# Performance work log

Measured on AMD Instinct MI355X. Metric: run time of the kernel, lower is better.

Reference implementation:

```python
import jax, jax.numpy as jnp
import numpy as np

D = 2048          # n_embd
F = 1408          # moe_inter_dim
E = 8             # n_routed_experts
TOPK = 2          # n_activated_experts
N_SHARED = 2
ROUTE_SCALE = 1.0


def setup_inputs() -> dict:
    key = jax.random.key(0)
    ks = jax.random.split(key, 8)
    s = 0.02
    x = jax.random.normal(ks[0], (2, 1024, D), dtype=jnp.float32)
    gate_w = jax.random.normal(ks[1], (D, E), dtype=jnp.float32) * s
    Fs = F * N_SHARED
    sw1 = jax.random.normal(ks[2], (D, Fs), dtype=jnp.float32) * s
    sw2 = jax.random.normal(ks[3], (Fs, D), dtype=jnp.float32) * s
    sw3 = jax.random.normal(ks[4], (D, Fs), dtype=jnp.float32) * s
    rw1 = jax.random.normal(ks[5], (E, D, F), dtype=jnp.float32) * s
    rw2 = jax.random.normal(ks[6], (E, F, D), dtype=jnp.float32) * s
    rw3 = jax.random.normal(ks[7], (E, D, F), dtype=jnp.float32) * s
    return {"x": x, "gate_w": gate_w, "sw1": sw1, "sw2": sw2, "sw3": sw3,
            "rw1": rw1, "rw2": rw2, "rw3": rw3}


def _swiglu(x, w1, w2, w3):
    return (jax.nn.silu(x @ w1) * (x @ w3)) @ w2


def reference(x, gate_w, sw1, sw2, sw3, rw1, rw2, rw3):
    B, T, _ = x.shape
    xf = x.reshape(-1, D)                       # [N, D]
    N = xf.shape[0]
    # shared experts (always applied)
    y = _swiglu(xf, sw1, sw2, sw3)              # [N, D]
    # gate: softmax scores, top-k (bias is None since n_embd != 7168; n_groups == 1)
    scores = jax.nn.softmax(xf @ gate_w, axis=-1)       # [N, E]
    weights, indices = jax.lax.top_k(scores, TOPK)       # gathered original scores
    weights = weights * ROUTE_SCALE
    # combine weights per (token, expert); zero for unassigned -> same math as
    # the per-expert gather/scatter loop in the original module
    cw = jnp.zeros((N, E), dtype=xf.dtype).at[jnp.arange(N)[:, None], indices].add(weights)
    for e in range(E):  # fixed small structural loop over experts
        h = _swiglu(xf, rw1[e], rw2[e], rw3[e])  # [N, D]
        y = y + cw[:, e:e + 1] * h
    return y.reshape(B, T, D)
```

## Files before the change

kernel.cpp:

```cpp
#include <hip/hip_runtime.h>
#include <hip/hip_bf16.h>
#include <math.h>

#define D_DIM 2048
#define F_DIM 1408
#define FS_DIM 2816
#define E_NUM 8
#define N_TOK 2048

typedef __attribute__((ext_vector_type(8))) short bf16x8;
typedef __attribute__((ext_vector_type(4))) float f32x4;

#define WAITVM(n) asm volatile("s_waitcnt vmcnt(" #n ")" ::: "memory")

__device__ inline short f2bf(float f) {
    __hip_bfloat16 h = __float2bfloat16(f);
    return *reinterpret_cast<short*>(&h);
}
__device__ inline float bf2f(short s) {
    __hip_bfloat16 h; *reinterpret_cast<short*>(&h) = s;
    return __bfloat162float(h);
}
__device__ inline float silu1(float v) { return v / (1.f + expf(-v)); }

__device__ inline void async_copy16(const void* g, void* l) {
    __builtin_amdgcn_global_load_lds(
        (const __attribute__((address_space(1))) void*)g,
        (__attribute__((address_space(3))) void*)l, 16, 0, 0);
}

__device__ inline void t64h(const float* in, short* out, int K, int N,
                            int kt, int nt, float (*tile)[65], int t)
{
    int k0 = kt * 64, n0 = nt * 64;
    int tr = t >> 4, tc4 = (t & 15) * 4;
#pragma unroll
    for (int i = 0; i < 4; ++i) {
        int r = tr + i * 16;
        float4 v = *reinterpret_cast<const float4*>(in + (size_t)(k0 + r) * N + n0 + tc4);
        tile[r][tc4 + 0] = v.x; tile[r][tc4 + 1] = v.y;
        tile[r][tc4 + 2] = v.z; tile[r][tc4 + 3] = v.w;
    }
    __syncthreads();
#pragma unroll
    for (int i = 0; i < 4; ++i) {
        int n = tr + i * 16;
        short4 s4;
        s4.x = f2bf(tile[tc4 + 0][n]);
        s4.y = f2bf(tile[tc4 + 1][n]);
        s4.z = f2bf(tile[tc4 + 2][n]);
        s4.w = f2bf(tile[tc4 + 3][n]);
        *reinterpret_cast<short4*>(out + (size_t)(n0 + n) * K + k0 + tc4) = s4;
    }
}

__global__ __launch_bounds__(256) void prep_kernel(
    const float* __restrict__ x, const float* __restrict__ gw,
    float* __restrict__ assign_w, int* __restrict__ expert_count,
    int* __restrict__ expert_list, short* __restrict__ Xb,
    const float* __restrict__ sw1, short* __restrict__ swt1,
    const float* __restrict__ sw3, short* __restrict__ swt3,
    const float* __restrict__ rw1, short* __restrict__ rwt1,
    const float* __restrict__ rw3, short* __restrict__ rwt3)
{
    __shared__ float tile[64][65];
    int bid = blockIdx.x;
    int tid = threadIdx.x;
    if (bid < 512) {
        int wid = bid * 4 + (tid >> 6);
        int lane = tid & 63;
        const float* xr = x + (size_t)wid * D_DIM;
        float p[E_NUM];
#pragma unroll
        for (int e = 0; e < E_NUM; ++e) p[e] = 0.f;
        for (int d = lane; d < D_DIM; d += 64) {
            float xv = xr[d];
            const float4* g = reinterpret_cast<const float4*>(gw + (size_t)d * E_NUM);
            float4 g0 = g[0], g1 = g[1];
            p[0] = fmaf(xv, g0.x, p[0]); p[1] = fmaf(xv, g0.y, p[1]);
            p[2] = fmaf(xv, g0.z, p[2]); p[3] = fmaf(xv, g0.w, p[3]);
            p[4] = fmaf(xv, g1.x, p[4]); p[5] = fmaf(xv, g1.y, p[5]);
            p[6] = fmaf(xv, g1.z, p[6]); p[7] = fmaf(xv, g1.w, p[7]);
        }
#pragma unroll
        for (int off = 32; off > 0; off >>= 1)
#pragma unroll
            for (int e = 0; e < E_NUM; ++e)
                p[e] += __shfl_xor(p[e], off, 64);
        if (lane == 0) {
            float m = p[0];
#pragma unroll
            for (int e = 1; e < E_NUM; ++e) m = fmaxf(m, p[e]);
            float s = 0.f, pr[E_NUM];
#pragma unroll
            for (int e = 0; e < E_NUM; ++e) { pr[e] = expf(p[e] - m); s += pr[e]; }
            float inv = 1.f / s;
#pragma unroll
            for (int e = 0; e < E_NUM; ++e) pr[e] *= inv;
            int i0 = 0;
#pragma unroll
            for (int e = 1; e < E_NUM; ++e) if (pr[e] > pr[i0]) i0 = e;
            int i1 = (i0 == 0) ? 1 : 0;
#pragma unroll
            for (int e = 0; e < E_NUM; ++e) if (e != i0 && pr[e] > pr[i1]) i1 = e;
            int s0 = wid * 2, s1 = wid * 2 + 1;
            assign_w[s0] = pr[i0];
            assign_w[s1] = pr[i1];
            int p0 = atomicAdd(&expert_count[i0], 1);
            expert_list[i0 * N_TOK + p0] = s0;
            int p1 = atomicAdd(&expert_count[i1], 1);
            expert_list[i1 * N_TOK + p1] = s1;
        }
    } else if (bid < 2560) {
        int i = ((bid - 512) * 256 + tid) * 8;
        float4 v0 = *reinterpret_cast<const float4*>(x + i);
        float4 v1 = *reinterpret_cast<const float4*>(x + i + 4);
        bf16x8 o;
        o[0] = f2bf(v0.x); o[1] = f2bf(v0.y); o[2] = f2bf(v0.z); o[3] = f2bf(v0.w);
        o[4] = f2bf(v1.x); o[5] = f2bf(v1.y); o[6] = f2bf(v1.z); o[7] = f2bf(v1.w);
        *reinterpret_cast<bf16x8*>(Xb + i) = o;
    } else if (bid < 3968) {
        int t = bid - 2560;
        t64h(sw1, swt1, D_DIM, FS_DIM, t % 32, t / 32, tile, tid);
    } else if (bid < 5376) {
        int t = bid - 3968;
        t64h(sw3, swt3, D_DIM, FS_DIM, t % 32, t / 32, tile, tid);
    } else if (bid < 11008) {
        int t = bid - 5376;
        int e = t / 704, r = t % 704;
        t64h(rw1 + (size_t)e * D_DIM * F_DIM, rwt1 + (size_t)e * F_DIM * D_DIM,
             D_DIM, F_DIM, r % 32, r / 32, tile, tid);
    } else {
        int t = bid - 11008;
        int e = t / 704, r = t % 704;
        t64h(rw3 + (size_t)e * D_DIM * F_DIM, rwt3 + (size_t)e * F_DIM * D_DIM,
             D_DIM, F_DIM, r % 32, r / 32, tile, tid);
    }
}

__global__ __launch_bounds__(512) void moe_in_kernel(
    const short* __restrict__ Xb,
    const short* __restrict__ swt1, const short* __restrict__ swt3, short* __restrict__ Hs,
    const short* __restrict__ rwt1, const short* __restrict__ rwt3, short* __restrict__ Hr,
    const int* __restrict__ expert_list, const int* __restrict__ expert_count,
    const float* __restrict__ sw2, short* __restrict__ swt2,
    const float* __restrict__ rw2, short* __restrict__ rwt2)
{
    __shared__ char SMEM[131072];
    int bid = blockIdx.x, tid = threadIdx.x;

    if (bid >= 896) {
        int t2 = (bid - 896) * 2 + (tid >> 8);
        int t256 = tid & 255;
        float (*tile)[65] = reinterpret_cast<float (*)[65]>(SMEM + (tid >> 8) * 16640);
        if (t2 < 1408) {
            t64h(sw2, swt2, FS_DIM, D_DIM, t2 % 44, t2 / 44, tile, t256);
        } else {
            int r = t2 - 1408;
            int e = r / 704, rr = r % 704;
            t64h(rw2 + (size_t)e * F_DIM * D_DIM, rwt2 + (size_t)e * D_DIM * F_DIM,
                 F_DIM, D_DIM, rr % 22, rr / 22, tile, t256);
        }
        return;
    }

    int xcd = bid & 7, qq = bid >> 3, mtile = qq & 7, gq = qq >> 3;
    int g = gq * 8 + xcd;
    if (g >= 110) return;
    bool gather;
    const short *W1, *W3;
    short* H;
    int ldH, n0, count;
    const int* list = nullptr;
    int m0 = mtile * 256;
    if (g < 22) {
        gather = false; count = N_TOK;
        W1 = swt1; W3 = swt3; H = Hs; ldH = FS_DIM; n0 = g * 128;
    } else {
        int g2 = g - 22, e = g2 / 11;
        n0 = (g2 % 11) * 128;
        gather = true;
        count = expert_count[e];
        if (m0 >= count) return;
        list = expert_list + e * N_TOK;
        W1 = rwt1 + (size_t)e * F_DIM * D_DIM;
        W3 = rwt3 + (size_t)e * F_DIM * D_DIM;
        H = Hr; ldH = F_DIM;
    }

    int l = tid & 63, w = tid >> 6;

    const char* aS[4];
#pragma unroll
    for (int j = 0; j < 4; ++j) {
        int u = j * 512 + tid, r = u >> 3, s = u & 7;
        int rr = m0 + r;
        int tok = gather ? ((rr < count) ? (list[rr] >> 1) : 0) : rr;
        aS[j] = (const char*)Xb + (size_t)tok * 4096 + ((s ^ (r & 7)) << 4);
    }
    const char *b1S[2], *b3S[2];
#pragma unroll
    for (int j = 0; j < 2; ++j) {
        int u = j * 512 + tid, r = u >> 3, s = u & 7;
        size_t off = (size_t)(n0 + r) * 4096 + ((s ^ (r & 7)) << 4);
        b1S[j] = (const char*)W1 + off;
        b3S[j] = (const char*)W3 + off;
    }

    auto STAGE = [&](int buf, int kb) {
        char* base = SMEM + buf * 65536;
#pragma unroll
        for (int j = 0; j < 4; ++j)
            async_copy16(aS[j] + kb, base + (j * 512 + tid) * 16);
#pragma unroll
        for (int j = 0; j < 2; ++j) {
            async_copy16(b1S[j] + kb, base + 32768 + (j * 512 + tid) * 16);
            async_copy16(b3S[j] + kb, base + 49152 + (j * 512 + tid) * 16);
        }
    };

    int wm = w >> 1, wn = w & 1, frow = l & 15, fkg = l >> 4;
    f32x4 acc1[4][4], acc3[4][4];
#pragma unroll
    for (int i = 0; i < 4; ++i)
#pragma unroll
        for (int j = 0; j < 4; ++j) { acc1[i][j] = (f32x4)0.f; acc3[i][j] = (f32x4)0.f; }

    STAGE(0, 0);
    int buf = 0;
    for (int it = 0; it < 32; ++it) {
        if (it < 31) { STAGE(buf ^ 1, (it + 1) << 7); WAITVM(8); }
        else         { WAITVM(0); }
        __builtin_amdgcn_s_barrier();
        const char* base = SMEM + buf * 65536;
#pragma unroll
        for (int kk = 0; kk < 2; ++kk) {
            bf16x8 af[4], b1f[4], b3f[4];
#pragma unroll
            for (int mf = 0; mf < 4; ++mf) {
                int r = wm * 64 + mf * 16 + frow;
                af[mf] = *reinterpret_cast<const bf16x8*>(
                    base + r * 128 + ((((kk << 2) | fkg) ^ (r & 7)) << 4));
            }
#pragma unroll
            for (int nf = 0; nf < 4; ++nf) {
                int r = wn * 64 + nf * 16 + frow;
                int so = (((kk << 2) | fkg) ^ (r & 7)) << 4;
                b1f[nf] = *reinterpret_cast<const bf16x8*>(base + 32768 + r * 128 + so);
                b3f[nf] = *reinterpret_cast<const bf16x8*>(base + 49152 + r * 128 + so);
            }
#pragma unroll
            for (int mf = 0; mf < 4; ++mf)
#pragma unroll
                for (int nf = 0; nf < 4; ++nf) {
                    acc1[mf][nf] = __builtin_amdgcn_mfma_f32_16x16x32_bf16(
                        af[mf], b1f[nf], acc1[mf][nf], 0, 0, 0);
                    acc3[mf][nf] = __builtin_amdgcn_mfma_f32_16x16x32_bf16(
                        af[mf], b3f[nf], acc3[mf][nf], 0, 0, 0);
                }
        }
        __builtin_amdgcn_s_barrier();
        buf ^= 1;
    }

#pragma unroll
    for (int mf = 0; mf < 4; ++mf) {
#pragma unroll
        for (int jj = 0; jj < 4; ++jj) {
            int rl = wm * 64 + mf * 16 + fkg * 4 + jj;
            int rr = m0 + rl;
            int s;
            if (gather) { if (rr >= count) continue; s = list[rr]; }
            else s = rr;
            short* hp = H + (size_t)s * ldH + n0 + wn * 64 + frow;
#pragma unroll
            for (int nf = 0; nf < 4; ++nf)
                hp[nf * 16] = f2bf(silu1(acc1[mf][nf][jj]) * acc3[mf][nf][jj]);
        }
    }
}

__global__ __launch_bounds__(512) void moe_out_kernel(
    const short* __restrict__ Hs, const short* __restrict__ swt2, float* __restrict__ Y,
    const short* __restrict__ Hr, const short* __restrict__ rwt2, short* __restrict__ H2,
    const int* __restrict__ expert_list, const int* __restrict__ expert_count)
{
    __shared__ char SMEM[98304];
    int bid = blockIdx.x, tid = threadIdx.x;
    int xcd = bid & 7, qq = bid >> 3, mtile = qq & 7, gq = qq >> 3;
    int g = gq * 8 + xcd;
    if (g >= 144) return;
    bool gather;
    const short *A, *B;
    int ldKb, NIT, n0, count;
    const int* list = nullptr;
    int m0 = mtile * 256;
    if (g < 16) {
        gather = false; count = N_TOK;
        A = Hs; ldKb = FS_DIM * 2; NIT = 44; B = swt2; n0 = g * 128;
    } else {
        int g2 = g - 16, e = g2 >> 4;
        n0 = (g2 & 15) * 128;
        gather = true;
        count = expert_count[e];
        if (m0 >= count) return;
        list = expert_list + e * N_TOK;
        A = Hr; ldKb = F_DIM * 2; NIT = 22;
        B = rwt2 + (size_t)e * D_DIM * F_DIM;
    }

    int l = tid & 63, w = tid >> 6;

    const char* aS[4];
#pragma unroll
    for (int j = 0; j < 4; ++j) {
        int u = j * 512 + tid, r = u >> 3, s = u & 7;
        int rr = m0 + r;
        int arow = gather ? ((rr < count) ? list[rr] : 0) : rr;
        aS[j] = (const char*)A + (size_t)arow * ldKb + ((s ^ (r & 7)) << 4);
    }
    const char* bS[2];
#pragma unroll
    for (int j = 0; j < 2; ++j) {
        int u = j * 512 + tid, r = u >> 3, s = u & 7;
        bS[j] = (const char*)B + (size_t)(n0 + r) * ldKb + ((s ^ (r & 7)) << 4);
    }

    auto STAGE = [&](int buf, int kb) {
        char* base = SMEM + buf * 49152;
#pragma unroll
        for (int j = 0; j < 4; ++j)
            async_copy16(aS[j] + kb, base + (j * 512 + tid) * 16);
#pragma unroll
        for (int j = 0; j < 2; ++j)
            async_copy16(bS[j] + kb, base + 32768 + (j * 512 + tid) * 16);
    };

    int wm = w >> 1, wn = w & 1, frow = l & 15, fkg = l >> 4;
    f32x4 acc[4][4];
#pragma unroll
    for (int i = 0; i < 4; ++i)
#pragma unroll
        for (int j = 0; j < 4; ++j) acc[i][j] = (f32x4)0.f;

    STAGE(0, 0);
    int buf = 0;
    for (int it = 0; it < NIT; ++it) {
        if (it + 1 < NIT) { STAGE(buf ^ 1, (it + 1) << 7); WAITVM(6); }
        else              { WAITVM(0); }
        __builtin_amdgcn_s_barrier();
        const char* base = SMEM + buf * 49152;
#pragma unroll
        for (int kk = 0; kk < 2; ++kk) {
            bf16x8 af[4], bf[4];
#pragma unroll
            for (int mf = 0; mf < 4; ++mf) {
                int r = wm * 64 + mf * 16 + frow;
                af[mf] = *reinterpret_cast<const bf16x8*>(
                    base + r * 128 + ((((kk << 2) | fkg) ^ (r & 7)) << 4));
            }
#pragma unroll
            for (int nf = 0; nf < 4; ++nf) {
                int r = wn * 64 + nf * 16 + frow;
                bf[nf] = *reinterpret_cast<const bf16x8*>(
                    base + 32768 + r * 128 + ((((kk << 2) | fkg) ^ (r & 7)) << 4));
            }
#pragma unroll
            for (int mf = 0; mf < 4; ++mf)
#pragma unroll
                for (int nf = 0; nf < 4; ++nf)
                    acc[mf][nf] = __builtin_amdgcn_mfma_f32_16x16x32_bf16(
                        af[mf], bf[nf], acc[mf][nf], 0, 0, 0);
        }
        __builtin_amdgcn_s_barrier();
        buf ^= 1;
    }

#pragma unroll
    for (int mf = 0; mf < 4; ++mf) {
#pragma unroll
        for (int jj = 0; jj < 4; ++jj) {
            int rl = wm * 64 + mf * 16 + fkg * 4 + jj;
            int rr = m0 + rl;
            int s;
            if (gather) { if (rr >= count) continue; s = list[rr]; }
            else s = rr;
            int col = n0 + wn * 64 + frow;
            if (!gather) {
                float* op = Y + (size_t)s * D_DIM + col;
#pragma unroll
                for (int nf = 0; nf < 4; ++nf)
                    op[nf * 16] = acc[mf][nf][jj];
            } else {
                short* op = H2 + (size_t)s * D_DIM + col;
#pragma unroll
                for (int nf = 0; nf < 4; ++nf)
                    op[nf * 16] = f2bf(acc[mf][nf][jj]);
            }
        }
    }
}

__global__ __launch_bounds__(256) void combine_kernel(
    float* __restrict__ Y, const short* __restrict__ H2,
    const float* __restrict__ assign_w)
{
    int tok = blockIdx.x, tid = threadIdx.x;
    float w0 = assign_w[2 * tok];
    float w1 = assign_w[2 * tok + 1];
    const short* h0 = H2 + (size_t)(2 * tok) * D_DIM + tid * 8;
    const short* h1 = h0 + D_DIM;
    bf16x8 a = *reinterpret_cast<const bf16x8*>(h0);
    bf16x8 b = *reinterpret_cast<const bf16x8*>(h1);
    float* y = Y + (size_t)tok * D_DIM + tid * 8;
    float4 y0 = *reinterpret_cast<float4*>(y);
    float4 y1 = *reinterpret_cast<float4*>(y + 4);
    y0.x = fmaf(w0, bf2f(a[0]), fmaf(w1, bf2f(b[0]), y0.x));
    y0.y = fmaf(w0, bf2f(a[1]), fmaf(w1, bf2f(b[1]), y0.y));
    y0.z = fmaf(w0, bf2f(a[2]), fmaf(w1, bf2f(b[2]), y0.z));
    y0.w = fmaf(w0, bf2f(a[3]), fmaf(w1, bf2f(b[3]), y0.w));
    y1.x = fmaf(w0, bf2f(a[4]), fmaf(w1, bf2f(b[4]), y1.x));
    y1.y = fmaf(w0, bf2f(a[5]), fmaf(w1, bf2f(b[5]), y1.y));
    y1.z = fmaf(w0, bf2f(a[6]), fmaf(w1, bf2f(b[6]), y1.z));
    y1.w = fmaf(w0, bf2f(a[7]), fmaf(w1, bf2f(b[7]), y1.w));
    *reinterpret_cast<float4*>(y) = y0;
    *reinterpret_cast<float4*>(y + 4) = y1;
}

extern "C" void kernel_launch(void* const* d_in, const int* in_sizes, int n_in,
                              void* d_out, int out_size, void* d_ws, size_t ws_size,
                              hipStream_t stream) {
    const float* x   = (const float*)d_in[0];
    const float* gw  = (const float*)d_in[1];
    const float* sw1 = (const float*)d_in[2];
    const float* sw2 = (const float*)d_in[3];
    const float* sw3 = (const float*)d_in[4];
    const float* rw1 = (const float*)d_in[5];
    const float* rw2 = (const float*)d_in[6];
    const float* rw3 = (const float*)d_in[7];
    float* Y = (float*)d_out;

    char* ws = (char*)d_ws;
    float* assign_w     = (float*)(ws);
    int*   expert_count = (int*)(ws + 16384);
    int*   expert_list  = (int*)(ws + 16384 + 256);

    const size_t XB_OFF   = 131072;
    const size_t SWT1_OFF = XB_OFF + 8388608ull;
    const size_t SWT3_OFF = SWT1_OFF + 11534336ull;
    const size_t SWT2_OFF = SWT3_OFF + 11534336ull;
    const size_t RWT1_OFF = SWT2_OFF + 11534336ull;
    const size_t RWT3_OFF = RWT1_OFF + 46137344ull;
    const size_t RWT2_OFF = RWT3_OFF + 46137344ull;
    const size_t HS_OFF   = RWT2_OFF + 46137344ull;
    const size_t HR_OFF   = HS_OFF + 11534336ull;
    const size_t H2_OFF   = HR_OFF + 11534336ull;

    short* Xb   = (short*)(ws + XB_OFF);
    short* swt1 = (short*)(ws + SWT1_OFF);
    short* swt3 = (short*)(ws + SWT3_OFF);
    short* swt2 = (short*)(ws + SWT2_OFF);
    short* rwt1 = (short*)(ws + RWT1_OFF);
    short* rwt3 = (short*)(ws + RWT3_OFF);
    short* rwt2 = (short*)(ws + RWT2_OFF);
    short* Hs   = (short*)(ws + HS_OFF);
    short* Hr   = (short*)(ws + HR_OFF);
    short* H2   = (short*)(ws + H2_OFF);

    hipMemsetAsync(expert_count, 0, E_NUM * sizeof(int), stream);

    prep_kernel<<<16640, 256, 0, stream>>>(
        x, gw, assign_w, expert_count, expert_list, Xb,
        sw1, swt1, sw3, swt3, rw1, rwt1, rw3, rwt3);

    moe_in_kernel<<<4416, 512, 0, stream>>>(
        Xb, swt1, swt3, Hs, rwt1, rwt3, Hr,
        expert_list, expert_count, sw2, swt2, rw2, rwt2);

    moe_out_kernel<<<1152, 512, 0, stream>>>(
        Hs, swt2, Y, Hr, rwt2, H2, expert_list, expert_count);

    combine_kernel<<<N_TOK, 256, 0, stream>>>(Y, H2, assign_w);
}
```

Before: 391.3 us.

## Switch MoE GEMMs to 4-stage K=32 pipeline with split-phase async loads

Both the gate/up and down-projection kernels move from a double-buffered K=64 loop to a four-buffer ring with K=32 steps and three stages prefetched ahead. Each step is split into two halves separated by a barrier, and the next stage's loads are issued between them so copies overlap the MFMA work. Warps are rearranged into a 2x4 grid of 128x32 subtiles, which changes the LDS fragment reuse pattern. s_setprio raises wave priority around the MFMA blocks. The aim is to hide global-load latency better, at the cost of twice as many barriers per unit of K and smaller LDS rows with a 4-way swizzle that may raise bank conflicts.

```diff
diff --git a/kernel.cpp b/kernel.cpp
--- a/kernel.cpp
+++ b/kernel.cpp
@@ -189,92 +189,99 @@
     }
 
     int l = tid & 63, w = tid >> 6;
-
-    const char* aS[4];
-#pragma unroll
-    for (int j = 0; j < 4; ++j) {
-        int u = j * 512 + tid, r = u >> 3, s = u & 7;
+    int wm = w >> 2, wn = w & 3, frow = l & 15, fkg = l >> 4;
+
+    const char* aS[2];
+#pragma unroll
+    for (int j = 0; j < 2; ++j) {
+        int u = j * 512 + tid, r = u >> 2, s = u & 3;
         int rr = m0 + r;
         int tok = gather ? ((rr < count) ? (list[rr] >> 1) : 0) : rr;
-        aS[j] = (const char*)Xb + (size_t)tok * 4096 + ((s ^ (r & 7)) << 4);
-    }
-    const char *b1S[2], *b3S[2];
-#pragma unroll
-    for (int j = 0; j < 2; ++j) {
-        int u = j * 512 + tid, r = u >> 3, s = u & 7;
-        size_t off = (size_t)(n0 + r) * 4096 + ((s ^ (r & 7)) << 4);
-        b1S[j] = (const char*)W1 + off;
-        b3S[j] = (const char*)W3 + off;
-    }
-
-    auto STAGE = [&](int buf, int kb) {
-        char* base = SMEM + buf * 65536;
-#pragma unroll
-        for (int j = 0; j < 4; ++j)
-            async_copy16(aS[j] + kb, base + (j * 512 + tid) * 16);
-#pragma unroll
-        for (int j = 0; j < 2; ++j) {
-            async_copy16(b1S[j] + kb, base + 32768 + (j * 512 + tid) * 16);
-            async_copy16(b3S[j] + kb, base + 49152 + (j * 512 + tid) * 16);
-        }
-    };
-
-    int wm = w >> 1, wn = w & 1, frow = l & 15, fkg = l >> 4;
-    f32x4 acc1[4][4], acc3[4][4];
-#pragma unroll
-    for (int i = 0; i < 4; ++i)
-#pragma unroll
-        for (int j = 0; j < 4; ++j) { acc1[i][j] = (f32x4)0.f; acc3[i][j] = (f32x4)0.f; }
-
-    STAGE(0, 0);
-    int buf = 0;
-    for (int it = 0; it < 32; ++it) {
-        if (it < 31) { STAGE(buf ^ 1, (it + 1) << 7); WAITVM(8); }
-        else         { WAITVM(0); }
+        aS[j] = (const char*)Xb + (size_t)tok * 4096 + ((s ^ (r & 3)) << 4);
+    }
+    int brr = tid >> 2, bss = tid & 3;
+    size_t boff = (size_t)(n0 + brr) * 4096 + ((bss ^ (brr & 3)) << 4);
+    const char* b1S = (const char*)W1 + boff;
+    const char* b3S = (const char*)W3 + boff;
+
+    f32x4 acc1[8][2], acc3[8][2];
+#pragma unroll
+    for (int i = 0; i < 8; ++i)
+#pragma unroll
+        for (int j = 0; j < 2; ++j) { acc1[i][j] = (f32x4)0.f; acc3[i][j] = (f32x4)0.f; }
+
+#pragma unroll
+    for (int p = 0; p < 3; ++p) {
+        char* base = SMEM + p * 32768;
+        int kb = p << 6;
+        async_copy16(aS[0] + kb, base + tid * 16);
+        async_copy16(aS[1] + kb, base + (512 + tid) * 16);
+        async_copy16(b1S + kb, base + 16384 + tid * 16);
+        async_copy16(b3S + kb, base + 24576 + tid * 16);
+    }
+
+    for (int t = 0; t < 64; ++t) {
+        const char* base = SMEM + (t & 3) * 32768;
+        int ts = (t + 3 < 64) ? (t + 3) : 63;
+        char* sbase = SMEM + ((t + 3) & 3) * 32768;
+        int skb = ts << 6;
+        WAITVM(8);
         __builtin_amdgcn_s_barrier();
-        const char* base = SMEM + buf * 65536;
-#pragma unroll
-        for (int kk = 0; kk < 2; ++kk) {
-            bf16x8 af[4], b1f[4], b3f[4];
-#pragma unroll
-            for (int mf = 0; mf < 4; ++mf) {
-                int r = wm * 64 + mf * 16 + frow;
-                af[mf] = *reinterpret_cast<const bf16x8*>(
-                    base + r * 128 + ((((kk << 2) | fkg) ^ (r & 7)) << 4));
-            }
-#pragma unroll
-            for (int nf = 0; nf < 4; ++nf) {
-                int r = wn * 64 + nf * 16 + frow;
-                int so = (((kk << 2) | fkg) ^ (r & 7)) << 4;
-                b1f[nf] = *reinterpret_cast<const bf16x8*>(base + 32768 + r * 128 + so);
-                b3f[nf] = *reinterpret_cast<const bf16x8*>(base + 49152 + r * 128 + so);
-            }
-#pragma unroll
-            for (int mf = 0; mf < 4; ++mf)
-#pragma unroll
-                for (int nf = 0; nf < 4; ++nf) {
-                    acc1[mf][nf] = __builtin_amdgcn_mfma_f32_16x16x32_bf16(
-                        af[mf], b1f[nf], acc1[mf][nf], 0, 0, 0);
-                    acc3[mf][nf] = __builtin_amdgcn_mfma_f32_16x16x32_bf16(
-                        af[mf], b3f[nf], acc3[mf][nf], 0, 0, 0);
-                }
-        }
+        bf16x8 af[8], bf[2];
+#pragma unroll
+        for (int mf = 0; mf < 8; ++mf) {
+            int r = wm * 128 + mf * 16 + frow;
+            af[mf] = *reinterpret_cast<const bf16x8*>(
+                base + r * 64 + ((fkg ^ (r & 3)) << 4));
+        }
+#pragma unroll
+        for (int nf = 0; nf < 2; ++nf) {
+            int rb = wn * 32 + nf * 16 + frow;
+            bf[nf] = *reinterpret_cast<const bf16x8*>(
+                base + 16384 + rb * 64 + ((fkg ^ (rb & 3)) << 4));
+        }
+        async_copy16(aS[0] + skb, sbase + tid * 16);
+        async_copy16(aS[1] + skb, sbase + (512 + tid) * 16);
+        __builtin_amdgcn_s_setprio(1);
+#pragma unroll
+        for (int mf = 0; mf < 8; ++mf)
+#pragma unroll
+            for (int nf = 0; nf < 2; ++nf)
+                acc1[mf][nf] = __builtin_amdgcn_mfma_f32_16x16x32_bf16(
+                    af[mf], bf[nf], acc1[mf][nf], 0, 0, 0);
+        __builtin_amdgcn_s_setprio(0);
         __builtin_amdgcn_s_barrier();
-        buf ^= 1;
-    }
-
-#pragma unroll
-    for (int mf = 0; mf < 4; ++mf) {
+#pragma unroll
+        for (int nf = 0; nf < 2; ++nf) {
+            int rb = wn * 32 + nf * 16 + frow;
+            bf[nf] = *reinterpret_cast<const bf16x8*>(
+                base + 24576 + rb * 64 + ((fkg ^ (rb & 3)) << 4));
+        }
+        async_copy16(b1S + skb, sbase + 16384 + tid * 16);
+        async_copy16(b3S + skb, sbase + 24576 + tid * 16);
+        __builtin_amdgcn_s_setprio(1);
+#pragma unroll
+        for (int mf = 0; mf < 8; ++mf)
+#pragma unroll
+            for (int nf = 0; nf < 2; ++nf)
+                acc3[mf][nf] = __builtin_amdgcn_mfma_f32_16x16x32_bf16(
+                    af[mf], bf[nf], acc3[mf][nf], 0, 0, 0);
+        __builtin_amdgcn_s_setprio(0);
+    }
+    WAITVM(0);
+
+#pragma unroll
+    for (int mf = 0; mf < 8; ++mf) {
 #pragma unroll
         for (int jj = 0; jj < 4; ++jj) {
-            int rl = wm * 64 + mf * 16 + fkg * 4 + jj;
+            int rl = wm * 128 + mf * 16 + fkg * 4 + jj;
             int rr = m0 + rl;
             int s;
             if (gather) { if (rr >= count) continue; s = list[rr]; }
             else s = rr;
-            short* hp = H + (size_t)s * ldH + n0 + wn * 64 + frow;
-#pragma unroll
-            for (int nf = 0; nf < 4; ++nf)
+            short* hp = H + (size_t)s * ldH + n0 + wn * 32 + frow;
+#pragma unroll
+            for (int nf = 0; nf < 2; ++nf)
                 hp[nf * 16] = f2bf(silu1(acc1[mf][nf][jj]) * acc3[mf][nf][jj]);
         }
     }
@@ -297,7 +304,7 @@
     int m0 = mtile * 256;
     if (g < 16) {
         gather = false; count = N_TOK;
-        A = Hs; ldKb = FS_DIM * 2; NIT = 44; B = swt2; n0 = g * 128;
+        A = Hs; ldKb = FS_DIM * 2; NIT = 88; B = swt2; n0 = g * 128;
     } else {
         int g2 = g - 16, e = g2 >> 4;
         n0 = (g2 & 15) * 128;
@@ -305,97 +312,100 @@
         count = expert_count[e];
         if (m0 >= count) return;
         list = expert_list + e * N_TOK;
-        A = Hr; ldKb = F_DIM * 2; NIT = 22;
+        A = Hr; ldKb = F_DIM * 2; NIT = 44;
         B = rwt2 + (size_t)e * D_DIM * F_DIM;
     }
 
     int l = tid & 63, w = tid >> 6;
-
-    const char* aS[4];
-#pragma unroll
-    for (int j = 0; j < 4; ++j) {
-        int u = j * 512 + tid, r = u >> 3, s = u & 7;
+    int wm = w >> 2, wn = w & 3, frow = l & 15, fkg = l >> 4;
+
+    const char* aS[2];
+#pragma unroll
+    for (int j = 0; j < 2; ++j) {
+        int u = j * 512 + tid, r = u >> 2, s = u & 3;
         int rr = m0 + r;
         int arow = gather ? ((rr < count) ? list[rr] : 0) : rr;
-        aS[j] = (const char*)A + (size_t)arow * ldKb + ((s ^ (r & 7)) << 4);
-    }
-    const char* bS[2];
-#pragma unroll
-    for (int j = 0; j < 2; ++j) {
-        int u = j * 512 + tid, r = u >> 3, s = u & 7;
-        bS[j] = (const char*)B + (size_t)(n0 + r) * ldKb + ((s ^ (r & 7)) << 4);
-    }
-
-    auto STAGE = [&](int buf, int kb) {
-        char* base = SMEM + buf * 49152;
-#pragma unroll
-        for (int j = 0; j < 4; ++j)
-            async_copy16(aS[j] + kb, base + (j * 512 + tid) * 16);
-#pragma unroll
-        for (int j = 0; j < 2; ++j)
-            async_copy16(bS[j] + kb, base + 32768 + (j * 512 + tid) * 16);
-    };
-
-    int wm = w >> 1, wn = w & 1, frow = l & 15, fkg = l >> 4;
-    f32x4 acc[4][4];
-#pragma unroll
-    for (int i = 0; i < 4; ++i)
-#pragma unroll
-        for (int j = 0; j < 4; ++j) acc[i][j] = (f32x4)0.f;
-
-    STAGE(0, 0);
-    int buf = 0;
-    for (int it = 0; it < NIT; ++it) {
-        if (it + 1 < NIT) { STAGE(buf ^ 1, (it + 1) << 7); WAITVM(6); }
-        else              { WAITVM(0); }
+        aS[j] = (const char*)A + (size_t)arow * ldKb + ((s ^ (r & 3)) << 4);
+    }
+    int brr = tid >> 2, bss = tid & 3;
+    const char* bS = (const char*)B + (size_t)(n0 + brr) * ldKb + ((bss ^ (brr & 3)) << 4);
+
+    f32x4 acc[8][2];
+#pragma unroll
+    for (int i = 0; i < 8; ++i)
+#pragma unroll
+        for (int j = 0; j < 2; ++j) acc[i][j] = (f32x4)0.f;
+
+#pragma unroll
+    for (int p = 0; p < 3; ++p) {
+        char* base = SMEM + p * 24576;
+        int kb = p << 6;
+        async_copy16(aS[0] + kb, base + tid * 16);
+        async_copy16(aS[1] + kb, base + (512 + tid) * 16);
+        async_copy16(bS + kb, base + 16384 + tid * 16);
+    }
+
+    for (int t = 0; t < NIT; ++t) {
+        const char* base = SMEM + (t & 3) * 24576;
+        int ts = (t + 3 < NIT) ? (t + 3) : (NIT - 1);
+        char* sbase = SMEM + ((t + 3) & 3) * 24576;
+        int skb = ts << 6;
+        WAITVM(6);
         __builtin_amdgcn_s_barrier();
-        const char* base = SMEM + buf * 49152;
-#pragma unroll
-        for (int kk = 0; kk < 2; ++kk) {
-            bf16x8 af[4], bf[4];
-#pragma unroll
-            for (int mf = 0; mf < 4; ++mf) {
-                int r = wm * 64 + mf * 16 + frow;
-                af[mf] = *reinterpret_cast<const bf16x8*>(
-                    base + r * 128 + ((((kk << 2) | fkg) ^ (r & 7)) << 4));
-            }
-#pragma unroll
-            for (int nf = 0; nf < 4; ++nf) {
-                int r = wn * 64 + nf * 16 + frow;
-                bf[nf] = *reinterpret_cast<const bf16x8*>(
-                    base + 32768 + r * 128 + ((((kk << 2) | fkg) ^ (r & 7)) << 4));
-            }
-#pragma unroll
-            for (int mf = 0; mf < 4; ++mf)
-#pragma unroll
-                for (int nf = 0; nf < 4; ++nf)
-                    acc[mf][nf] = __builtin_amdgcn_mfma_f32_16x16x32_bf16(
-                        af[mf], bf[nf], acc[mf][nf], 0, 0, 0);
-        }
+        bf16x8 af[8], bf0, bf1;
+#pragma unroll
+        for (int mf = 0; mf < 8; ++mf) {
+            int r = wm * 128 + mf * 16 + frow;
+            af[mf] = *reinterpret_cast<const bf16x8*>(
+                base + r * 64 + ((fkg ^ (r & 3)) << 4));
+        }
+        {
+            int rb = wn * 32 + frow;
+            bf0 = *reinterpret_cast<const bf16x8*>(
+                base + 16384 + rb * 64 + ((fkg ^ (rb & 3)) << 4));
+        }
+        async_copy16(aS[0] + skb, sbase + tid * 16);
+        async_copy16(aS[1] + skb, sbase + (512 + tid) * 16);
+        __builtin_amdgcn_s_setprio(1);
+#pragma unroll
+        for (int mf = 0; mf < 8; ++mf)
+            acc[mf][0] = __builtin_amdgcn_mfma_f32_16x16x32_bf16(
+                af[mf], bf0, acc[mf][0], 0, 0, 0);
+        __builtin_amdgcn_s_setprio(0);
         __builtin_amdgcn_s_barrier();
-        buf ^= 1;
-    }
-
-#pragma unroll
-    for (int mf = 0; mf < 4; ++mf) {
+        {
+            int rb = wn * 32 + 16 + frow;
+            bf1 = *reinterpret_cast<const bf16x8*>(
+                base + 16384 + rb * 64 + ((fkg ^ (rb & 3)) << 4));
+        }
+        async_copy16(bS + skb, sbase + 16384 + tid * 16);
+        __builtin_amdgcn_s_setprio(1);
+#pragma unroll
+        for (int mf = 0; mf < 8; ++mf)
+            acc[mf][1] = __builtin_amdgcn_mfma_f32_16x16x32_bf16(
+                af[mf], bf1, acc[mf][1], 0, 0, 0);
+        __builtin_amdgcn_s_setprio(0);
+    }
+    WAITVM(0);
+
+#pragma unroll
+    for (int mf = 0; mf < 8; ++mf) {
 #pragma unroll
         for (int jj = 0; jj < 4; ++jj) {
-            int rl = wm * 64 + mf * 16 + fkg * 4 + jj;
+            int rl = wm * 128 + mf * 16 + fkg * 4 + jj;
             int rr = m0 + rl;
             int s;
             if (gather) { if (rr >= count) continue; s = list[rr]; }
             else s = rr;
-            int col = n0 + wn * 64 + frow;
+            int col = n0 + wn * 32 + frow;
             if (!gather) {
                 float* op = Y + (size_t)s * D_DIM + col;
-#pragma unroll
-                for (int nf = 0; nf < 4; ++nf)
-                    op[nf * 16] = acc[mf][nf][jj];
+                op[0] = acc[mf][0][jj];
+                op[16] = acc[mf][1][jj];
             } else {
                 short* op = H2 + (size_t)s * D_DIM + col;
-#pragma unroll
-                for (int nf = 0; nf < 4; ++nf)
-                    op[nf * 16] = f2bf(acc[mf][nf][jj]);
+                op[0] = f2bf(acc[mf][0][jj]);
+                op[16] = f2bf(acc[mf][1][jj]);
             }
         }
     }
```

Result: slower. 412.0 us (+5.3%).

## Shrink GEMM tiles, use 3-stage BK=32 pipeline with single barrier

Applied to the files above, without the earlier changes.

Both MoE GEMM kernels move from 512-thread 256-row tiles with a 2-stage BK=64 double buffer to 256-thread 128-row tiles (and 64-wide N tiles for the gate/up GEMM). They use a 3-stage BK=32 LDS ring with a new 4-chunk swizzle and one barrier per iteration. MFMA sections are wrapped in s_setprio. The goal is smaller LDS per block, higher occupancy and more blocks for load balance across the uneven per-expert counts, with deeper prefetch to hide global load latency. In exchange, each block reuses less data, which raises global and L2 traffic, and there are twice as many loop iterations to pay overhead on.

```diff
diff --git a/kernel.cpp b/kernel.cpp
--- a/kernel.cpp
+++ b/kernel.cpp
@@ -28,6 +28,8 @@
         (const __attribute__((address_space(1))) void*)g,
         (__attribute__((address_space(3))) void*)l, 16, 0, 0);
 }
+
+#define SWZ(r, s) ((((s) ^ (((r) >> 1) & 3)) & 3) << 4)
 
 __device__ inline void t64h(const float* in, short* out, int K, int N,
                             int kt, int nt, float (*tile)[65], int t)
@@ -138,7 +140,7 @@
     }
 }
 
-__global__ __launch_bounds__(512) void moe_in_kernel(
+__global__ __launch_bounds__(256) void moe_in_kernel(
     const short* __restrict__ Xb,
     const short* __restrict__ swt1, const short* __restrict__ swt3, short* __restrict__ Hs,
     const short* __restrict__ rwt1, const short* __restrict__ rwt3, short* __restrict__ Hr,
@@ -146,39 +148,38 @@
     const float* __restrict__ sw2, short* __restrict__ swt2,
     const float* __restrict__ rw2, short* __restrict__ rwt2)
 {
-    __shared__ char SMEM[131072];
+    __shared__ char SMEM[49152];
     int bid = blockIdx.x, tid = threadIdx.x;
 
-    if (bid >= 896) {
-        int t2 = (bid - 896) * 2 + (tid >> 8);
-        int t256 = tid & 255;
-        float (*tile)[65] = reinterpret_cast<float (*)[65]>(SMEM + (tid >> 8) * 16640);
+    if (bid >= 3584) {
+        int t2 = bid - 3584;
+        float (*tile)[65] = reinterpret_cast<float (*)[65]>(SMEM);
         if (t2 < 1408) {
-            t64h(sw2, swt2, FS_DIM, D_DIM, t2 % 44, t2 / 44, tile, t256);
+            t64h(sw2, swt2, FS_DIM, D_DIM, t2 % 44, t2 / 44, tile, tid);
         } else {
             int r = t2 - 1408;
             int e = r / 704, rr = r % 704;
             t64h(rw2 + (size_t)e * F_DIM * D_DIM, rwt2 + (size_t)e * D_DIM * F_DIM,
-                 F_DIM, D_DIM, rr % 22, rr / 22, tile, t256);
+                 F_DIM, D_DIM, rr % 22, rr / 22, tile, tid);
         }
         return;
     }
 
-    int xcd = bid & 7, qq = bid >> 3, mtile = qq & 7, gq = qq >> 3;
+    int xcd = bid & 7, qq = bid >> 3, mtile = qq & 15, gq = qq >> 4;
     int g = gq * 8 + xcd;
-    if (g >= 110) return;
+    if (g >= 220) return;
     bool gather;
     const short *W1, *W3;
     short* H;
     int ldH, n0, count;
     const int* list = nullptr;
-    int m0 = mtile * 256;
-    if (g < 22) {
+    int m0 = mtile * 128;
+    if (g < 44) {
         gather = false; count = N_TOK;
-        W1 = swt1; W3 = swt3; H = Hs; ldH = FS_DIM; n0 = g * 128;
+        W1 = swt1; W3 = swt3; H = Hs; ldH = FS_DIM; n0 = g * 64;
     } else {
-        int g2 = g - 22, e = g2 / 11;
-        n0 = (g2 % 11) * 128;
+        int g2 = g - 44, e = g2 / 22;
+        n0 = (g2 % 22) * 64;
         gather = true;
         count = expert_count[e];
         if (m0 >= count) return;
@@ -189,79 +190,76 @@
     }
 
     int l = tid & 63, w = tid >> 6;
-
-    const char* aS[4];
-#pragma unroll
-    for (int j = 0; j < 4; ++j) {
-        int u = j * 512 + tid, r = u >> 3, s = u & 7;
+    int wm = w >> 1, wn = w & 1, frow = l & 15, fkg = l >> 4;
+
+    const char* aS[2];
+#pragma unroll
+    for (int j = 0; j < 2; ++j) {
+        int u = j * 256 + tid, r = u >> 2, s = u & 3;
         int rr = m0 + r;
         int tok = gather ? ((rr < count) ? (list[rr] >> 1) : 0) : rr;
-        aS[j] = (const char*)Xb + (size_t)tok * 4096 + ((s ^ (r & 7)) << 4);
-    }
-    const char *b1S[2], *b3S[2];
-#pragma unroll
-    for (int j = 0; j < 2; ++j) {
-        int u = j * 512 + tid, r = u >> 3, s = u & 7;
-        size_t off = (size_t)(n0 + r) * 4096 + ((s ^ (r & 7)) << 4);
-        b1S[j] = (const char*)W1 + off;
-        b3S[j] = (const char*)W3 + off;
-    }
-
-    auto STAGE = [&](int buf, int kb) {
-        char* base = SMEM + buf * 65536;
-#pragma unroll
-        for (int j = 0; j < 4; ++j)
-            async_copy16(aS[j] + kb, base + (j * 512 + tid) * 16);
-#pragma unroll
-        for (int j = 0; j < 2; ++j) {
-            async_copy16(b1S[j] + kb, base + 32768 + (j * 512 + tid) * 16);
-            async_copy16(b3S[j] + kb, base + 49152 + (j * 512 + tid) * 16);
-        }
-    };
-
-    int wm = w >> 1, wn = w & 1, frow = l & 15, fkg = l >> 4;
-    f32x4 acc1[4][4], acc3[4][4];
+        aS[j] = (const char*)Xb + (size_t)tok * 4096 + SWZ(r, s);
+    }
+    int brr = tid >> 2, bss = tid & 3;
+    size_t boff = (size_t)(n0 + brr) * 4096 + SWZ(brr, bss);
+    const char* b1S = (const char*)W1 + boff;
+    const char* b3S = (const char*)W3 + boff;
+
+    f32x4 acc1[4][2], acc3[4][2];
 #pragma unroll
     for (int i = 0; i < 4; ++i)
 #pragma unroll
-        for (int j = 0; j < 4; ++j) { acc1[i][j] = (f32x4)0.f; acc3[i][j] = (f32x4)0.f; }
-
-    STAGE(0, 0);
-    int buf = 0;
-    for (int it = 0; it < 32; ++it) {
-        if (it < 31) { STAGE(buf ^ 1, (it + 1) << 7); WAITVM(8); }
-        else         { WAITVM(0); }
+        for (int j = 0; j < 2; ++j) { acc1[i][j] = (f32x4)0.f; acc3[i][j] = (f32x4)0.f; }
+
+#pragma unroll
+    for (int p = 0; p < 2; ++p) {
+        char* base = SMEM + p * 16384;
+        int kb = p << 6;
+        async_copy16(aS[0] + kb, base + tid * 16);
+        async_copy16(aS[1] + kb, base + (256 + tid) * 16);
+        async_copy16(b1S + kb, base + 8192 + tid * 16);
+        async_copy16(b3S + kb, base + 12288 + tid * 16);
+    }
+
+    const int NIT = 64;
+    for (int t = 0; t < NIT; ++t) {
+        const char* base = SMEM + (t % 3) * 16384;
+        WAITVM(4);
         __builtin_amdgcn_s_barrier();
-        const char* base = SMEM + buf * 65536;
-#pragma unroll
-        for (int kk = 0; kk < 2; ++kk) {
-            bf16x8 af[4], b1f[4], b3f[4];
-#pragma unroll
-            for (int mf = 0; mf < 4; ++mf) {
-                int r = wm * 64 + mf * 16 + frow;
-                af[mf] = *reinterpret_cast<const bf16x8*>(
-                    base + r * 128 + ((((kk << 2) | fkg) ^ (r & 7)) << 4));
+        {
+            int ts = (t + 2 < NIT) ? (t + 2) : (NIT - 1);
+            char* sbase = SMEM + ((t + 2) % 3) * 16384;
+            int skb = ts << 6;
+            async_copy16(aS[0] + skb, sbase + tid * 16);
+            async_copy16(aS[1] + skb, sbase + (256 + tid) * 16);
+            async_copy16(b1S + skb, sbase + 8192 + tid * 16);
+            async_copy16(b3S + skb, sbase + 12288 + tid * 16);
+        }
+        bf16x8 af[4], b1f[2], b3f[2];
+#pragma unroll
+        for (int mf = 0; mf < 4; ++mf) {
+            int r = wm * 64 + mf * 16 + frow;
+            af[mf] = *reinterpret_cast<const bf16x8*>(base + r * 64 + SWZ(r, fkg));
+        }
+#pragma unroll
+        for (int nf = 0; nf < 2; ++nf) {
+            int rb = wn * 32 + nf * 16 + frow;
+            b1f[nf] = *reinterpret_cast<const bf16x8*>(base + 8192 + rb * 64 + SWZ(rb, fkg));
+            b3f[nf] = *reinterpret_cast<const bf16x8*>(base + 12288 + rb * 64 + SWZ(rb, fkg));
+        }
+        __builtin_amdgcn_s_setprio(1);
+#pragma unroll
+        for (int mf = 0; mf < 4; ++mf)
+#pragma unroll
+            for (int nf = 0; nf < 2; ++nf) {
+                acc1[mf][nf] = __builtin_amdgcn_mfma_f32_16x16x32_bf16(
+                    af[mf], b1f[nf], acc1[mf][nf], 0, 0, 0);
+                acc3[mf][nf] = __builtin_amdgcn_mfma_f32_16x16x32_bf16(
+                    af[mf], b3f[nf], acc3[mf][nf], 0, 0, 0);
             }
-#pragma unroll
-            for (int nf = 0; nf < 4; ++nf) {
-                int r = wn * 64 + nf * 16 + frow;
-                int so = (((kk << 2) | fkg) ^ (r & 7)) << 4;
-                b1f[nf] = *reinterpret_cast<const bf16x8*>(base + 32768 + r * 128 + so);
-                b3f[nf] = *reinterpret_cast<const bf16x8*>(base + 49152 + r * 128 + so);
-            }
-#pragma unroll
-            for (int mf = 0; mf < 4; ++mf)
-#pragma unroll
-                for (int nf = 0; nf < 4; ++nf) {
-                    acc1[mf][nf] = __builtin_amdgcn_mfma_f32_16x16x32_bf16(
-                        af[mf], b1f[nf], acc1[mf][nf], 0, 0, 0);
-                    acc3[mf][nf] = __builtin_amdgcn_mfma_f32_16x16x32_bf16(
-                        af[mf], b3f[nf], acc3[mf][nf], 0, 0, 0);
-                }
-        }
-        __builtin_amdgcn_s_barrier();
-        buf ^= 1;
-    }
+        __builtin_amdgcn_s_setprio(0);
+    }
+    WAITVM(0);
 
 #pragma unroll
     for (int mf = 0; mf < 4; ++mf) {
@@ -272,32 +270,32 @@
             int s;
             if (gather) { if (rr >= count) continue; s = list[rr]; }
             else s = rr;
-            short* hp = H + (size_t)s * ldH + n0 + wn * 64 + frow;
-#pragma unroll
-            for (int nf = 0; nf < 4; ++nf)
+            short* hp = H + (size_t)s * ldH + n0 + wn * 32 + frow;
+#pragma unroll
+            for (int nf = 0; nf < 2; ++nf)
                 hp[nf * 16] = f2bf(silu1(acc1[mf][nf][jj]) * acc3[mf][nf][jj]);
         }
     }
 }
 
-__global__ __launch_bounds__(512) void moe_out_kernel(
+__global__ __launch_bounds__(256) void moe_out_kernel(
     const short* __restrict__ Hs, const short* __restrict__ swt2, float* __restrict__ Y,
     const short* __restrict__ Hr, const short* __restrict__ rwt2, short* __restrict__ H2,
     const int* __restrict__ expert_list, const int* __restrict__ expert_count)
 {
-    __shared__ char SMEM[98304];
+    __shared__ char SMEM[49152];
     int bid = blockIdx.x, tid = threadIdx.x;
-    int xcd = bid & 7, qq = bid >> 3, mtile = qq & 7, gq = qq >> 3;
+    int xcd = bid & 7, qq = bid >> 3, mtile = qq & 15, gq = qq >> 4;
     int g = gq * 8 + xcd;
     if (g >= 144) return;
     bool gather;
     const short *A, *B;
     int ldKb, NIT, n0, count;
     const int* list = nullptr;
-    int m0 = mtile * 256;
+    int m0 = mtile * 128;
     if (g < 16) {
         gather = false; count = N_TOK;
-        A = Hs; ldKb = FS_DIM * 2; NIT = 44; B = swt2; n0 = g * 128;
+        A = Hs; ldKb = FS_DIM * 2; NIT = 88; B = swt2; n0 = g * 128;
     } else {
         int g2 = g - 16, e = g2 >> 4;
         n0 = (g2 & 15) * 128;
@@ -305,76 +303,78 @@
         count = expert_count[e];
         if (m0 >= count) return;
         list = expert_list + e * N_TOK;
-        A = Hr; ldKb = F_DIM * 2; NIT = 22;
+        A = Hr; ldKb = F_DIM * 2; NIT = 44;
         B = rwt2 + (size_t)e * D_DIM * F_DIM;
     }
 
     int l = tid & 63, w = tid >> 6;
-
-    const char* aS[4];
-#pragma unroll
-    for (int j = 0; j < 4; ++j) {
-        int u = j * 512 + tid, r = u >> 3, s = u & 7;
+    int wm = w >> 1, wn = w & 1, frow = l & 15, fkg = l >> 4;
+
+    const char* aS[2];
+#pragma unroll
+    for (int j = 0; j < 2; ++j) {
+        int u = j * 256 + tid, r = u >> 2, s = u & 3;
         int rr = m0 + r;
         int arow = gather ? ((rr < count) ? list[rr] : 0) : rr;
-        aS[j] = (const char*)A + (size_t)arow * ldKb + ((s ^ (r & 7)) << 4);
+        aS[j] = (const char*)A + (size_t)arow * ldKb + SWZ(r, s);
     }
     const char* bS[2];
 #pragma unroll
     for (int j = 0; j < 2; ++j) {
-        int u = j * 512 + tid, r = u >> 3, s = u & 7;
-        bS[j] = (const char*)B + (size_t)(n0 + r) * ldKb + ((s ^ (r & 7)) << 4);
-    }
-
-    auto STAGE = [&](int buf, int kb) {
-        char* base = SMEM + buf * 49152;
-#pragma unroll
-        for (int j = 0; j < 4; ++j)
-            async_copy16(aS[j] + kb, base + (j * 512 + tid) * 16);
-#pragma unroll
-        for (int j = 0; j < 2; ++j)
-            async_copy16(bS[j] + kb, base + 32768 + (j * 512 + tid) * 16);
-    };
-
-    int wm = w >> 1, wn = w & 1, frow = l & 15, fkg = l >> 4;
+        int u = j * 256 + tid, r = u >> 2, s = u & 3;
+        bS[j] = (const char*)B + (size_t)(n0 + r) * ldKb + SWZ(r, s);
+    }
+
     f32x4 acc[4][4];
 #pragma unroll
     for (int i = 0; i < 4; ++i)
 #pragma unroll
         for (int j = 0; j < 4; ++j) acc[i][j] = (f32x4)0.f;
 
-    STAGE(0, 0);
-    int buf = 0;
-    for (int it = 0; it < NIT; ++it) {
-        if (it + 1 < NIT) { STAGE(buf ^ 1, (it + 1) << 7); WAITVM(6); }
-        else              { WAITVM(0); }
+#pragma unroll
+    for (int p = 0; p < 2; ++p) {
+        char* base = SMEM + p * 16384;
+        int kb = p << 6;
+        async_copy16(aS[0] + kb, base + tid * 16);
+        async_copy16(aS[1] + kb, base + (256 + tid) * 16);
+        async_copy16(bS[0] + kb, base + 8192 + tid * 16);
+        async_copy16(bS[1] + kb, base + 8192 + (256 + tid) * 16);
+    }
+
+    for (int t = 0; t < NIT; ++t) {
+        const char* base = SMEM + (t % 3) * 16384;
+        WAITVM(4);
         __builtin_amdgcn_s_barrier();
-        const char* base = SMEM + buf * 49152;
-#pragma unroll
-        for (int kk = 0; kk < 2; ++kk) {
-            bf16x8 af[4], bf[4];
-#pragma unroll
-            for (int mf = 0; mf < 4; ++mf) {
-                int r = wm * 64 + mf * 16 + frow;
-                af[mf] = *reinterpret_cast<const bf16x8*>(
-                    base + r * 128 + ((((kk << 2) | fkg) ^ (r & 7)) << 4));
-            }
-#pragma unroll
-            for (int nf = 0; nf < 4; ++nf) {
-                int r = wn * 64 + nf * 16 + frow;
-                bf[nf] = *reinterpret_cast<const bf16x8*>(
-                    base + 32768 + r * 128 + ((((kk << 2) | fkg) ^ (r & 7)) << 4));
-            }
-#pragma unroll
-            for (int mf = 0; mf < 4; ++mf)
-#pragma unroll
-                for (int nf = 0; nf < 4; ++nf)
-                    acc[mf][nf] = __builtin_amdgcn_mfma_f32_16x16x32_bf16(
-                        af[mf], bf[nf], acc[mf][nf], 0, 0, 0);
-        }
-        __builtin_amdgcn_s_barrier();
-        buf ^= 1;
-    }
+        {
+            int ts = (t + 2 < NIT) ? (t + 2) : (NIT - 1);
+            char* sbase = SMEM + ((t + 2) % 3) * 16384;
+            int skb = ts << 6;
+            async_copy16(aS[0] + skb, sbase + tid * 16);
+            async_copy16(aS[1] + skb, sbase + (256 + tid) * 16);
+            async_copy16(bS[0] + skb, sbase + 8192 + tid * 16);
+            async_copy16(bS[1] + skb, sbase + 8192 + (256 + tid) * 16);
+        }
+        bf16x8 af[4], bf[4];
+#pragma unroll
+        for (int mf = 0; mf < 4; ++mf) {
+            int r = wm * 64 + mf * 16 + frow;
+            af[mf] = *reinterpret_cast<const bf16x8*>(base + r * 64 + SWZ(r, fkg));
+        }
+#pragma unroll
+        for (int nf = 0; nf < 4; ++nf) {
+            int rb = wn * 64 + nf * 16 + frow;
+            bf[nf] = *reinterpret_cast<const bf16x8*>(base + 8192 + rb * 64 + SWZ(rb, fkg));
+        }
+        __builtin_amdgcn_s_setprio(1);
+#pragma unroll
+        for (int mf = 0; mf < 4; ++mf)
+#pragma unroll
+            for (int nf = 0; nf < 4; ++nf)
+                acc[mf][nf] = __builtin_amdgcn_mfma_f32_16x16x32_bf16(
+                    af[mf], bf[nf], acc[mf][nf], 0, 0, 0);
+        __builtin_amdgcn_s_setprio(0);
+    }
+    WAITVM(0);
 
 #pragma unroll
     for (int mf = 0; mf < 4; ++mf) {
@@ -473,11 +473,11 @@
         x, gw, assign_w, expert_count, expert_list, Xb,
         sw1, swt1, sw3, swt3, rw1, rwt1, rw3, rwt3);
 
-    moe_in_kernel<<<4416, 512, 0, stream>>>(
+    moe_in_kernel<<<10624, 256, 0, stream>>>(
         Xb, swt1, swt3, Hs, rwt1, rwt3, Hr,
         expert_list, expert_count, sw2, swt2, rw2, rwt2);
 
-    moe_out_kernel<<<1152, 512, 0, stream>>>(
+    moe_out_kernel<<<2304, 256, 0, stream>>>(
         Hs, swt2, Y, Hr, rwt2, H2, expert_list, expert_count);
 
     combine_kernel<<<N_TOK, 256, 0, stream>>>(Y, H2, assign_w);
```

After: 368.6 us. -5.8%, faster.
